# Kernel optimization log

Hardware: AMD Instinct MI355X
Metric: run time of the kernel (lower is better)

Reference implementation:

```python
import jax, jax.numpy as jnp
import numpy as np

N_HEADS = 8
STATE_TEMP = 0.5


def layer_norm(x, g, b, eps=1e-5):
    m = x.mean(-1, keepdims=True)
    v = ((x - m) ** 2).mean(-1, keepdims=True)
    return (x - m) / jnp.sqrt(v + eps) * g + b


def setup_inputs() -> dict:
    key = jax.random.key(0)
    ks = jax.random.split(key, 16)
    B, G, H, C, S, M, L = 2048, 10000, 256, 16, 32, 100, 3
    f32 = jnp.float32
    rn = lambda k, shape, scale: jax.random.normal(k, shape, f32) * scale
    return {
        'x': rn(ks[0], (B, G), 1.0),
        'enc_w1': rn(ks[1], (G, 2 * H), 1.0 / np.sqrt(G)),
        'enc_b1': jnp.zeros((2 * H,), f32),
        'enc_ln_g': jnp.ones((2 * H,), f32),
        'enc_ln_b': jnp.zeros((2 * H,), f32),
        'enc_w2': rn(ks[2], (2 * H, H), 1.0 / np.sqrt(2 * H)),
        'enc_b2': jnp.zeros((H,), f32),
        'mod_assign': rn(ks[3], (M, G), 1.0),
        'mod_inter': rn(ks[4], (M, M), 0.1) + jnp.eye(M, dtype=f32),
        'qkv_w': rn(ks[5], (L, H, 3 * H), 1.0 / np.sqrt(H)),
        'qkv_b': jnp.zeros((L, 3 * H), f32),
        'out_w': rn(ks[6], (L, H, H), 1.0 / np.sqrt(H)),
        'out_b': jnp.zeros((L, H), f32),
        'ln_g': jnp.ones((L, H), f32),
        'ln_b': jnp.zeros((L, H), f32),
        'prototypes': rn(ks[7], (S, H), 1.0),
        'clf_w1': rn(ks[8], (H, H // 2), 1.0 / np.sqrt(H)),
        'clf_b1': jnp.zeros((H // 2,), f32),
        'clf_w2': rn(ks[9], (H // 2, C), 1.0 / np.sqrt(H // 2)),
        'clf_b2': jnp.zeros((C,), f32),
        'marker_weights': jax.random.uniform(ks[10], (C, G), f32),
    }


def reference(x, enc_w1, enc_b1, enc_ln_g, enc_ln_b, enc_w2, enc_b2,
              mod_assign, mod_inter, qkv_w, qkv_b, out_w, out_b, ln_g, ln_b,
              prototypes, clf_w1, clf_b1, clf_w2, clf_b2, marker_weights):
    B = x.shape[0]
    Hd = enc_w2.shape[1]
    hd = Hd // N_HEADS
    # --- gene encoder (Linear -> LN -> ReLU -> Linear), dropout off (eval) ---
    h = jax.nn.relu(layer_norm(x @ enc_w1 + enc_b1, enc_ln_g, enc_ln_b))
    gene_features = h @ enc_w2 + enc_b2  # [B, Hd]
    # --- gene regulatory module (only sparsity_loss feeds the output dict) ---
    module_weights = jax.nn.softmax(mod_assign, axis=1)  # [M, G]
    sparsity_loss = jnp.mean(jnp.abs(module_weights)) * 0.01
    # --- stacked biological attention over seq_len N = 1 ---
    f = gene_features[:, None, :]  # [B, 1, Hd]
    for i in range(qkv_w.shape[0]):
        residual = f
        qkv = (f @ qkv_w[i] + qkv_b[i]).reshape(B, 1, 3, N_HEADS, hd)
        qkv = qkv.transpose(2, 0, 3, 1, 4)  # [3, B, nh, 1, hd]
        q, k, v = qkv[0], qkv[1], qkv[2]
        # N=1 != n_genes so the interaction-mask branch is skipped
        attn = jax.nn.softmax((q @ k.swapaxes(-2, -1)) * hd ** -0.5, axis=-1)
        o = (attn @ v).swapaxes(1, 2).reshape(B, 1, Hd)
        o = o @ out_w[i] + out_b[i]
        f = layer_norm(o + residual, ln_g[i], ln_b[i])
    feats = f[:, 0]  # [B, Hd]
    # --- soft assignment to cell-state prototypes via cosine similarity ---
    fn = jnp.linalg.norm(feats, axis=-1, keepdims=True)  # [B, 1]
    pn = jnp.linalg.norm(prototypes, axis=-1)            # [S]
    sim = (feats @ prototypes.T) / jnp.maximum(fn * pn[None, :], 1e-8)
    state_weights = jax.nn.softmax(sim / STATE_TEMP, axis=1)
    cell_states = state_weights @ prototypes  # [B, Hd]
    # --- classifier head ---
    logits = jax.nn.relu(cell_states @ clf_w1 + clf_b1) @ clf_w2 + clf_b2
    # --- eval-mode marker scores from buffer ---
    C, G = marker_weights.shape
    marker_scores = jnp.broadcast_to(marker_weights[None], (B, C, G))
    denom = jnp.maximum(jnp.sum(jnp.abs(marker_weights), axis=1, keepdims=True), 1e-12)
    marker_importance = marker_weights / denom
    return (logits, cell_states, sparsity_loss, marker_scores, marker_importance)
```

## Files before the change

kernel.cpp:

```cpp
#include <hip/hip_runtime.h>
#include <stdint.h>

#define GG 10000
#define H2 512
#define KP 10240
#define KZ 8
#define KCH 1280
#define KSTEPS 40

#define O_CS 32768L
#define O_SP 557056L
#define O_MS 557057L
#define O_MI 328237057L

typedef __attribute__((ext_vector_type(8))) short v8s;
typedef __attribute__((ext_vector_type(4))) float v4f;
typedef __attribute__((ext_vector_type(4))) unsigned short u16x4;
typedef __attribute__((ext_vector_type(8))) unsigned short u16x8;

__device__ __forceinline__ unsigned short bf16_rne(float f){
  unsigned u = __float_as_uint(f);
  u += 0x7fffu + ((u>>16)&1u);
  return (unsigned short)(u>>16);
}
__device__ __forceinline__ float bf16_f(unsigned short h){
  return __uint_as_float(((unsigned)h)<<16);
}

#define GL16(g,l) __builtin_amdgcn_global_load_lds( \
    (__attribute__((address_space(1))) void*)(uintptr_t)(g), \
    (__attribute__((address_space(3))) void*)(l), 16, 0, 0)

__global__ __launch_bounds__(256) void k_prep(
    const float* __restrict__ x, const float* __restrict__ w1,
    const float* __restrict__ qkv_w, const float* __restrict__ qkv_b,
    const float* __restrict__ out_w, const float* __restrict__ out_b,
    unsigned short* __restrict__ xh, unsigned short* __restrict__ wth,
    unsigned short* __restrict__ wtl, float* __restrict__ Wc, float* __restrict__ bc){
  __shared__ unsigned T[64][65];
  __shared__ float As[64][36], WsT[64][36];
  const int bid = blockIdx.x, tid = threadIdx.x;
  if (bid < 20480){
    int idx = bid*256 + tid;
    int row = idx / (KP/4);
    int k = (idx - row*(KP/4))*4;
    float4 v = make_float4(0.f,0.f,0.f,0.f);
    if (k < GG) v = *(const float4*)(x + (long)row*GG + k);
    float c[4] = {v.x,v.y,v.z,v.w};
    u16x4 hv;
    #pragma unroll
    for (int j=0;j<4;j++) hv[j] = bf16_rne(c[j]);
    *(u16x4*)(xh + (long)row*KP + k) = hv;
  } else if (bid < 21760){
    int b = bid - 20480;
    int k0 = (b%160)*64, n0 = (b/160)*64;
    {
      int kr = tid>>2, nc = (tid&3)*16;
      int kk = k0 + kr;
      #pragma unroll
      for (int j=0;j<16;j+=4){
        float4 v = make_float4(0.f,0.f,0.f,0.f);
        if (kk < GG) v = *(const float4*)(w1 + (long)kk*H2 + n0 + nc + j);
        float c[4] = {v.x,v.y,v.z,v.w};
        #pragma unroll
        for (int jj=0;jj<4;jj++){
          unsigned short h = bf16_rne(c[jj]);
          unsigned short l = bf16_rne(c[jj] - bf16_f(h));
          T[kr][nc+j+jj] = (unsigned)h | ((unsigned)l<<16);
        }
      }
    }
    __syncthreads();
    {
      int n = tid>>2, kc = (tid&3)*16;
      u16x8 h0, h1, l0, l1;
      #pragma unroll
      for (int j=0;j<8;j++){
        unsigned a = T[kc+j][n];
        unsigned bb = T[kc+8+j][n];
        h0[j] = (unsigned short)(a & 0xffffu); l0[j] = (unsigned short)(a>>16);
        h1[j] = (unsigned short)(bb & 0xffffu); l1[j] = (unsigned short)(bb>>16);
      }
      long off = (long)(n0+n)*KP + k0 + kc;
      *(u16x8*)(wth+off)   = h0; *(u16x8*)(wth+off+8) = h1;
      *(u16x8*)(wtl+off)   = l0; *(u16x8*)(wtl+off+8) = l1;
    }
  } else if (bid < 21808){
    int b = bid - 21760;
    const int z = b>>4, bx = (b&15)>>2, by = b&3;
    const float* A = qkv_w + (long)z*196608 + 512;
    const float* W = out_w + (long)z*65536;
    float* C = Wc + (long)z*65536;
    const int tx = tid&15, ty = tid>>4;
    const int ar = tid>>2, ak = (tid&3)*8;
    const int wr2 = tid>>3, wc2 = (tid&7)*8;
    float acc[4][4];
    #pragma unroll
    for (int i=0;i<4;i++)
      #pragma unroll
      for (int j=0;j<4;j++) acc[i][j] = 0.f;
    for (int kb=0; kb<256; kb+=32){
      float4 a0 = *(const float4*)(A + (long)(bx*64+ar)*768 + kb + ak);
      float4 a1 = *(const float4*)(A + (long)(bx*64+ar)*768 + kb + ak + 4);
      float4 w0 = *(const float4*)(W + (long)(kb+wr2)*256 + by*64 + wc2);
      float4 w1v= *(const float4*)(W + (long)(kb+wr2)*256 + by*64 + wc2 + 4);
      __syncthreads();
      *(float4*)&As[ar][ak]   = a0;
      *(float4*)&As[ar][ak+4] = a1;
      float cw[8] = {w0.x,w0.y,w0.z,w0.w,w1v.x,w1v.y,w1v.z,w1v.w};
      #pragma unroll
      for (int jj=0;jj<8;jj++) WsT[wc2+jj][wr2] = cw[jj];
      __syncthreads();
      #pragma unroll
      for (int k4=0;k4<8;k4++){
        float4 av[4], wv[4];
        #pragma unroll
        for (int i=0;i<4;i++) av[i] = *(const float4*)&As[ty + i*16][k4*4];
        #pragma unroll
        for (int j=0;j<4;j++) wv[j] = *(const float4*)&WsT[tx + j*16][k4*4];
        #pragma unroll
        for (int i=0;i<4;i++)
          #pragma unroll
          for (int j=0;j<4;j++)
            acc[i][j] += av[i].x*wv[j].x + av[i].y*wv[j].y + av[i].z*wv[j].z + av[i].w*wv[j].w;
      }
    }
    #pragma unroll
    for (int i=0;i<4;i++){
      int r = bx*64 + ty + i*16;
      #pragma unroll
      for (int j=0;j<4;j++)
        C[(long)r*256 + by*64 + tx + j*16] = acc[i][j];
    }
  } else {
    int i = bid - 21808;
    float acc = out_b[i*256 + tid];
    const float* wo = out_w + (long)i*65536;
    const float* qb = qkv_b + i*768 + 512;
    for (int j=0;j<256;j++) acc += qb[j]*wo[j*256+tid];
    bc[i*256+tid] = acc;
  }
}

__global__ __launch_bounds__(256) void k_gemm1(
    const unsigned short* __restrict__ xh,
    const unsigned short* __restrict__ wth, const unsigned short* __restrict__ wtl,
    float* __restrict__ pc){
  __shared__ unsigned short Ah[4096], Bh[4096], Bl[4096];
  const int tid = threadIdx.x;
  const int wid = tid>>6, lane = tid&63;
  const int bm = blockIdx.x, bn = blockIdx.y, kz = blockIdx.z;
  const int c0 = wid*2, c1 = c0+1;
  const int srow = lane>>2;
  const int sk8 = (lane&3)*8;
  const long kb0 = (long)kz*KCH + sk8;
  const long rA0 = (long)(bm*128 + c0*16 + srow)*KP + kb0;
  const long rA1 = (long)(bm*128 + c1*16 + srow)*KP + kb0;
  const long rB0 = (long)(bn*128 + c0*16 + srow)*KP + kb0;
  const long rB1 = (long)(bn*128 + c1*16 + srow)*KP + kb0;
  const unsigned short* pAh0 = xh + rA0;  const unsigned short* pAh1 = xh + rA1;
  const unsigned short* pBh0 = wth + rB0; const unsigned short* pBh1 = wth + rB1;
  const unsigned short* pBl0 = wtl + rB0; const unsigned short* pBl1 = wtl + rB1;
  unsigned short* dAh0 = &Ah[c0*512]; unsigned short* dAh1 = &Ah[c1*512];
  unsigned short* dBh0 = &Bh[c0*512]; unsigned short* dBh1 = &Bh[c1*512];
  unsigned short* dBl0 = &Bl[c0*512]; unsigned short* dBl1 = &Bl[c1*512];
  const int wr = wid>>1, wc = wid&1;
  const int fr = lane&15, fq = lane>>4;
  v4f acc[4][4];
  #pragma unroll
  for (int m=0;m<4;m++)
    #pragma unroll
    for (int n=0;n<4;n++){ v4f z = {0.f,0.f,0.f,0.f}; acc[m][n] = z; }

  for (int s=0; s<KSTEPS; ++s){
    GL16(pAh0, dAh0); GL16(pAh1, dAh1);
    GL16(pBh0, dBh0); GL16(pBh1, dBh1);
    GL16(pBl0, dBl0); GL16(pBl1, dBl1);
    pAh0 += 32; pAh1 += 32;
    pBh0 += 32; pBh1 += 32; pBl0 += 32; pBl1 += 32;
    __syncthreads();
    v8s ah[4], bh[4], bl[4];
    #pragma unroll
    for (int m=0;m<4;m++)
      ah[m] = *(const v8s*)&Ah[(wr*64 + m*16 + fr)*32 + fq*8];
    #pragma unroll
    for (int n=0;n<4;n++){
      int off = (wc*64 + n*16 + fr)*32 + fq*8;
      bh[n] = *(const v8s*)&Bh[off];
      bl[n] = *(const v8s*)&Bl[off];
    }
    #pragma unroll
    for (int m=0;m<4;m++)
      #pragma unroll
      for (int n=0;n<4;n++){
        acc[m][n] = __builtin_amdgcn_mfma_f32_16x16x32_bf16(ah[m], bh[n], acc[m][n], 0,0,0);
        acc[m][n] = __builtin_amdgcn_mfma_f32_16x16x32_bf16(ah[m], bl[n], acc[m][n], 0,0,0);
      }
    __syncthreads();
  }
  float* op = pc + (long)kz*(2048L*512L);
  #pragma unroll
  for (int m=0;m<4;m++){
    #pragma unroll
    for (int n=0;n<4;n++){
      int col = bn*128 + wc*64 + n*16 + fr;
      #pragma unroll
      for (int r=0;r<4;r++){
        int row = bm*128 + wr*64 + m*16 + fq*4 + r;
        op[(long)row*512 + col] = acc[m][n][r];
      }
    }
  }
}

__global__ __launch_bounds__(256) void k_reduce_ln(const float* __restrict__ pc,
    const float* __restrict__ b1, const float* __restrict__ g, const float* __restrict__ b,
    float* __restrict__ t1){
  __shared__ float red[8];
  int row = blockIdx.x, tid = threadIdx.x;
  long base = (long)row*512;
  float v0 = b1[tid], v1 = b1[tid+256];
  #pragma unroll
  for (int kz=0;kz<KZ;kz++){
    v0 += pc[(long)kz*1048576 + base + tid];
    v1 += pc[(long)kz*1048576 + base + tid + 256];
  }
  float s = v0+v1, q = v0*v0 + v1*v1;
  #pragma unroll
  for (int off=32; off; off>>=1){ s += __shfl_xor(s, off); q += __shfl_xor(q, off); }
  if ((tid&63)==0){ red[tid>>6] = s; red[4+(tid>>6)] = q; }
  __syncthreads();
  float sum = red[0]+red[1]+red[2]+red[3];
  float ssq = red[4]+red[5]+red[6]+red[7];
  float mean = sum*(1.f/512.f);
  float var  = ssq*(1.f/512.f) - mean*mean;
  float rstd = rsqrtf(var + 1e-5f);
  float r0 = (v0-mean)*rstd*g[tid]     + b[tid];
  float r1 = (v1-mean)*rstd*g[tid+256] + b[tid+256];
  t1[base+tid]     = fmaxf(r0, 0.f);
  t1[base+tid+256] = fmaxf(r1, 0.f);
}

__global__ __launch_bounds__(256) void k_gemm_f32(
    const float* __restrict__ A, int lda,
    const float* __restrict__ W, int ldw,
    const float* __restrict__ bias,
    float* __restrict__ C, int ldo, int K){
  __shared__ float As[64][36];
  __shared__ float WsT[64][36];
  const int tid = threadIdx.x;
  const int bx = blockIdx.x, by = blockIdx.y;
  const int tx = tid&15, ty = tid>>4;
  const int ar = tid>>2, ak = (tid&3)*8;
  const int wr2 = tid>>3, wc2 = (tid&7)*8;
  float acc[4][4];
  #pragma unroll
  for (int i=0;i<4;i++)
    #pragma unroll
    for (int j=0;j<4;j++) acc[i][j] = 0.f;
  for (int kb=0; kb<K; kb+=32){
    float4 a0 = *(const float4*)(A + (long)(bx*64+ar)*lda + kb + ak);
    float4 a1 = *(const float4*)(A + (long)(bx*64+ar)*lda + kb + ak + 4);
    float4 w0 = *(const float4*)(W + (long)(kb+wr2)*ldw + by*64 + wc2);
    float4 w1v= *(const float4*)(W + (long)(kb+wr2)*ldw + by*64 + wc2 + 4);
    __syncthreads();
    *(float4*)&As[ar][ak]   = a0;
    *(float4*)&As[ar][ak+4] = a1;
    float cw[8] = {w0.x,w0.y,w0.z,w0.w,w1v.x,w1v.y,w1v.z,w1v.w};
    #pragma unroll
    for (int jj=0;jj<8;jj++) WsT[wc2+jj][wr2] = cw[jj];
    __syncthreads();
    #pragma unroll
    for (int k4=0;k4<8;k4++){
      float4 av[4], wv[4];
      #pragma unroll
      for (int i=0;i<4;i++) av[i] = *(const float4*)&As[ty + i*16][k4*4];
      #pragma unroll
      for (int j=0;j<4;j++) wv[j] = *(const float4*)&WsT[tx + j*16][k4*4];
      #pragma unroll
      for (int i=0;i<4;i++)
        #pragma unroll
        for (int j=0;j<4;j++)
          acc[i][j] += av[i].x*wv[j].x + av[i].y*wv[j].y + av[i].z*wv[j].z + av[i].w*wv[j].w;
    }
  }
  #pragma unroll
  for (int i=0;i<4;i++){
    int r = bx*64 + ty + i*16;
    #pragma unroll
    for (int j=0;j<4;j++){
      int c = by*64 + tx + j*16;
      C[(long)r*ldo + c] = acc[i][j] + bias[c];
    }
  }
}

__global__ __launch_bounds__(256) void k_add_ln(const float* __restrict__ o,
    const float* __restrict__ res, const float* __restrict__ g, const float* __restrict__ b,
    float* __restrict__ fout){
  __shared__ float red[8];
  int row = blockIdx.x, tid = threadIdx.x;
  long base = (long)row*256;
  float x = o[base+tid] + res[base+tid];
  float s = x, q = x*x;
  #pragma unroll
  for (int off=32; off; off>>=1){ s += __shfl_xor(s, off); q += __shfl_xor(q, off); }
  if ((tid&63)==0){ red[tid>>6] = s; red[4+(tid>>6)] = q; }
  __syncthreads();
  float sum = red[0]+red[1]+red[2]+red[3];
  float ssq = red[4]+red[5]+red[6]+red[7];
  float mean = sum*(1.f/256.f);
  float var  = ssq*(1.f/256.f) - mean*mean;
  float rstd = rsqrtf(var + 1e-5f);
  fout[base+tid] = (x-mean)*rstd*g[tid] + b[tid];
}

__global__ __launch_bounds__(256) void k_head(const float* __restrict__ o,
    const float* __restrict__ res, const float* __restrict__ g3, const float* __restrict__ b3,
    const float* __restrict__ protos, const float* __restrict__ w1, const float* __restrict__ b1,
    const float* __restrict__ w2, const float* __restrict__ b2,
    float* __restrict__ logits, float* __restrict__ cs_out){
  __shared__ float ff[256], csb[256], hid[128], simr[32], pnl[32], sw[32], red[8];
  int row = blockIdx.x, tid = threadIdx.x;
  long base = (long)row*256;
  float xx = o[base+tid] + res[base+tid];
  {
    float s0 = xx, q0 = xx*xx;
    #pragma unroll
    for (int off=32; off; off>>=1){ s0 += __shfl_xor(s0, off); q0 += __shfl_xor(q0, off); }
    if ((tid&63)==0){ red[tid>>6] = s0; red[4+(tid>>6)] = q0; }
  }
  __syncthreads();
  float fv;
  {
    float sum = red[0]+red[1]+red[2]+red[3];
    float ssq = red[4]+red[5]+red[6]+red[7];
    float mean = sum*(1.f/256.f);
    float var  = ssq*(1.f/256.f) - mean*mean;
    float rstd = rsqrtf(var + 1e-5f);
    fv = (xx-mean)*rstd*g3[tid] + b3[tid];
  }
  ff[tid] = fv;
  __syncthreads();
  float s = fv*fv;
  #pragma unroll
  for (int off=32; off; off>>=1) s += __shfl_xor(s, off);
  if ((tid&63)==0) red[tid>>6] = s;
  __syncthreads();
  float fn = sqrtf(red[0]+red[1]+red[2]+red[3]);
  int p = tid>>3, e = tid&7;
  float d = 0.f, q = 0.f;
  for (int k=e*32; k<e*32+32; k++){ float pv = protos[p*256+k]; d += ff[k]*pv; q += pv*pv; }
  d += __shfl_xor(d,1); q += __shfl_xor(q,1);
  d += __shfl_xor(d,2); q += __shfl_xor(q,2);
  d += __shfl_xor(d,4); q += __shfl_xor(q,4);
  if (e==0){ simr[p] = d; pnl[p] = sqrtf(q); }
  __syncthreads();
  if (tid < 64){
    float z = (tid<32) ? (2.f*simr[tid]/fmaxf(fn*pnl[tid], 1e-8f)) : -3e38f;
    float m = z;
    #pragma unroll
    for (int off=16; off; off>>=1) m = fmaxf(m, __shfl_xor(m, off));
    float ev = (tid<32) ? expf(z - m) : 0.f;
    float sm = ev;
    #pragma unroll
    for (int off=16; off; off>>=1) sm += __shfl_xor(sm, off);
    if (tid<32) sw[tid] = ev/sm;
  }
  __syncthreads();
  float cs = 0.f;
  #pragma unroll 8
  for (int pp=0;pp<32;pp++) cs += sw[pp]*protos[pp*256+tid];
  cs_out[(long)row*256+tid] = cs;
  csb[tid] = cs;
  __syncthreads();
  if (tid<128){
    float hv = b1[tid];
    for (int k=0;k<256;k++) hv += csb[k]*w1[k*128+tid];
    hid[tid] = fmaxf(hv, 0.f);
  }
  __syncthreads();
  if (tid<16){
    float lv = b2[tid];
    for (int j=0;j<128;j++) lv += hid[j]*w2[j*16+tid];
    logits[(long)row*16+tid] = lv;
  }
}

__global__ __launch_bounds__(256) void k_fill_marker(const float* __restrict__ mw,
    float* __restrict__ out){
  __shared__ float red[4];
  int b = blockIdx.y;
  int t = blockIdx.x*256 + threadIdx.x;
  if (b == 2048){
    int c = blockIdx.x, tid = threadIdx.x;
    if (c >= 16) return;
    if (c==0 && tid==0) out[O_SP] = 0.01f/10000.0f;
    float s = 0.f;
    for (int g0=tid; g0<10000; g0+=256) s += fabsf(mw[c*10000+g0]);
    #pragma unroll
    for (int off=32; off; off>>=1) s += __shfl_xor(s, off);
    if ((tid&63)==0) red[tid>>6] = s;
    __syncthreads();
    float inv = 1.f/fmaxf(red[0]+red[1]+red[2]+red[3], 1e-12f);
    for (int g0=tid; g0<10000; g0+=256)
      out[O_MI + (long)c*10000 + g0] = mw[c*10000+g0]*inv;
    return;
  }
  float* base = out + O_MS + (long)b*160000;
  if (t < 40000){
    int i = 4*t;
    float4 A  = *(const float4*)(mw + i);
    float4 Bv = (i+4 < 160000) ? *(const float4*)(mw + i + 4) : *(const float4*)(mw);
    float4 v = make_float4(A.w, Bv.x, Bv.y, Bv.z);
    if (b == 2047 && t == 39999){
      base[159999] = A.w;
    } else {
      *(float4*)(base + 3 + i) = v;
    }
  }
  if (b==0 && t<3) base[t] = mw[t];
}

extern "C" void kernel_launch(void* const* d_in, const int* in_sizes, int n_in,
                              void* d_out, int out_size, void* d_ws, size_t ws_size,
                              hipStream_t stream){
  const float* x        = (const float*)d_in[0];
  const float* enc_w1   = (const float*)d_in[1];
  const float* enc_b1   = (const float*)d_in[2];
  const float* enc_ln_g = (const float*)d_in[3];
  const float* enc_ln_b = (const float*)d_in[4];
  const float* enc_w2   = (const float*)d_in[5];
  const float* enc_b2   = (const float*)d_in[6];
  const float* qkv_w    = (const float*)d_in[9];
  const float* qkv_b    = (const float*)d_in[10];
  const float* out_w    = (const float*)d_in[11];
  const float* out_b    = (const float*)d_in[12];
  const float* ln_g     = (const float*)d_in[13];
  const float* ln_b     = (const float*)d_in[14];
  const float* protos   = (const float*)d_in[15];
  const float* clf_w1   = (const float*)d_in[16];
  const float* clf_b1   = (const float*)d_in[17];
  const float* clf_w2   = (const float*)d_in[18];
  const float* clf_b2   = (const float*)d_in[19];
  const float* mw       = (const float*)d_in[20];
  float* out = (float*)d_out;

  char* scr = (char*)(((uintptr_t)d_out + O_MS*4 + 255) & ~(uintptr_t)255);
  unsigned short* xh  = (unsigned short*)(scr);
  unsigned short* wth = (unsigned short*)(scr + 83886080L);
  unsigned short* wtl = (unsigned short*)(scr + 94371840L);
  float* pc = (float*)(scr + 104857600L);
  float* t1 = (float*)(scr + 138412032L);
  float* f0 = (float*)(scr + 142606336L);
  float* f1 = (float*)(scr + 144703488L);
  float* ob = (float*)(scr + 146800640L);
  float* Wc = (float*)(scr + 148897792L);
  float* bc = (float*)(scr + 149684224L);

  k_prep     <<<21811, 256, 0, stream>>>(x, enc_w1, qkv_w, qkv_b, out_w, out_b,
                                         xh, wth, wtl, Wc, bc);
  k_gemm1    <<<dim3(16, 4, KZ), 256, 0, stream>>>(xh, wth, wtl, pc);
  k_reduce_ln<<<2048, 256, 0, stream>>>(pc, enc_b1, enc_ln_g, enc_ln_b, t1);
  k_gemm_f32 <<<dim3(32, 4), 256, 0, stream>>>(t1, 512, enc_w2, 256, enc_b2, f0, 256, 512);
  const float* fin = f0; float* fo = f1;
  for (int i=0;i<2;i++){
    k_gemm_f32<<<dim3(32,4), 256, 0, stream>>>(fin, 256, Wc + (long)i*65536, 256,
                                               bc + i*256, ob, 256, 256);
    k_add_ln  <<<2048, 256, 0, stream>>>(ob, fin, ln_g + i*256, ln_b + i*256, fo);
    const float* tmp = fo; fo = (float*)fin; fin = tmp;
  }
  k_gemm_f32<<<dim3(32,4), 256, 0, stream>>>(fin, 256, Wc + 2L*65536, 256,
                                             bc + 2*256, ob, 256, 256);
  k_head<<<2048, 256, 0, stream>>>(ob, fin, ln_g + 512, ln_b + 512,
                                   protos, clf_w1, clf_b1, clf_w2, clf_b2,
                                   out, out + O_CS);
  k_fill_marker<<<dim3(157, 2049), 256, 0, stream>>>(mw, out);
}
```

Before: 527.0 us.

## Triple-buffer LDS tiles in gemm1 with async global-to-LDS prefetch pipeline

The encoder GEMM now keeps three LDS buffers per operand and issues direct global-to-LDS loads three K-steps ahead. Partial s_waitcnt vmcnt values replace the full syncthreads drain, so global memory latency overlaps with MFMA work. LDS use triples, which may lower occupancy. Correctness depends on the vmcnt counts matching the six loads issued per stage.

```diff
diff --git a/kernel.cpp b/kernel.cpp
--- a/kernel.cpp
+++ b/kernel.cpp
@@ -146,7 +146,7 @@
     const unsigned short* __restrict__ xh,
     const unsigned short* __restrict__ wth, const unsigned short* __restrict__ wtl,
     float* __restrict__ pc){
-  __shared__ unsigned short Ah[4096], Bh[4096], Bl[4096];
+  __shared__ unsigned short Ah[3][4096], Bh[3][4096], Bl[3][4096];
   const int tid = threadIdx.x;
   const int wid = tid>>6, lane = tid&63;
   const int bm = blockIdx.x, bn = blockIdx.y, kz = blockIdx.z;
@@ -154,16 +154,13 @@
   const int srow = lane>>2;
   const int sk8 = (lane&3)*8;
   const long kb0 = (long)kz*KCH + sk8;
-  const long rA0 = (long)(bm*128 + c0*16 + srow)*KP + kb0;
-  const long rA1 = (long)(bm*128 + c1*16 + srow)*KP + kb0;
-  const long rB0 = (long)(bn*128 + c0*16 + srow)*KP + kb0;
-  const long rB1 = (long)(bn*128 + c1*16 + srow)*KP + kb0;
-  const unsigned short* pAh0 = xh + rA0;  const unsigned short* pAh1 = xh + rA1;
-  const unsigned short* pBh0 = wth + rB0; const unsigned short* pBh1 = wth + rB1;
-  const unsigned short* pBl0 = wtl + rB0; const unsigned short* pBl1 = wtl + rB1;
-  unsigned short* dAh0 = &Ah[c0*512]; unsigned short* dAh1 = &Ah[c1*512];
-  unsigned short* dBh0 = &Bh[c0*512]; unsigned short* dBh1 = &Bh[c1*512];
-  unsigned short* dBl0 = &Bl[c0*512]; unsigned short* dBl1 = &Bl[c1*512];
+  const unsigned short* pA0 = xh  + (long)(bm*128 + c0*16 + srow)*KP + kb0;
+  const unsigned short* pA1 = xh  + (long)(bm*128 + c1*16 + srow)*KP + kb0;
+  const unsigned short* pH0 = wth + (long)(bn*128 + c0*16 + srow)*KP + kb0;
+  const unsigned short* pH1 = wth + (long)(bn*128 + c1*16 + srow)*KP + kb0;
+  const unsigned short* pL0 = wtl + (long)(bn*128 + c0*16 + srow)*KP + kb0;
+  const unsigned short* pL1 = wtl + (long)(bn*128 + c1*16 + srow)*KP + kb0;
+  const int d0 = c0*512, d1 = c1*512;
   const int wr = wid>>1, wc = wid&1;
   const int fr = lane&15, fq = lane>>4;
   v4f acc[4][4];
@@ -172,22 +169,28 @@
     #pragma unroll
     for (int n=0;n<4;n++){ v4f z = {0.f,0.f,0.f,0.f}; acc[m][n] = z; }
 
+#define STAGE(d, s) do{ long o=(long)(s)*32; \
+    GL16(pA0+o, &Ah[d][d0]); GL16(pA1+o, &Ah[d][d1]); \
+    GL16(pH0+o, &Bh[d][d0]); GL16(pH1+o, &Bh[d][d1]); \
+    GL16(pL0+o, &Bl[d][d0]); GL16(pL1+o, &Bl[d][d1]); }while(0)
+
+  STAGE(0, 0); STAGE(1, 1); STAGE(2, 2);
+  int cur = 0;
   for (int s=0; s<KSTEPS; ++s){
-    GL16(pAh0, dAh0); GL16(pAh1, dAh1);
-    GL16(pBh0, dBh0); GL16(pBh1, dBh1);
-    GL16(pBl0, dBl0); GL16(pBl1, dBl1);
-    pAh0 += 32; pAh1 += 32;
-    pBh0 += 32; pBh1 += 32; pBl0 += 32; pBl1 += 32;
-    __syncthreads();
+    if (s <= KSTEPS-3)      asm volatile("s_waitcnt vmcnt(12)" ::: "memory");
+    else if (s == KSTEPS-2) asm volatile("s_waitcnt vmcnt(6)"  ::: "memory");
+    else                    asm volatile("s_waitcnt vmcnt(0)"  ::: "memory");
+    __builtin_amdgcn_s_barrier();
+    __builtin_amdgcn_sched_barrier(0);
     v8s ah[4], bh[4], bl[4];
     #pragma unroll
     for (int m=0;m<4;m++)
-      ah[m] = *(const v8s*)&Ah[(wr*64 + m*16 + fr)*32 + fq*8];
+      ah[m] = *(const v8s*)&Ah[cur][(wr*64 + m*16 + fr)*32 + fq*8];
     #pragma unroll
     for (int n=0;n<4;n++){
       int off = (wc*64 + n*16 + fr)*32 + fq*8;
-      bh[n] = *(const v8s*)&Bh[off];
-      bl[n] = *(const v8s*)&Bl[off];
+      bh[n] = *(const v8s*)&Bh[cur][off];
+      bl[n] = *(const v8s*)&Bl[cur][off];
     }
     #pragma unroll
     for (int m=0;m<4;m++)
@@ -196,8 +199,12 @@
         acc[m][n] = __builtin_amdgcn_mfma_f32_16x16x32_bf16(ah[m], bh[n], acc[m][n], 0,0,0);
         acc[m][n] = __builtin_amdgcn_mfma_f32_16x16x32_bf16(ah[m], bl[n], acc[m][n], 0,0,0);
       }
-    __syncthreads();
-  }
+    __builtin_amdgcn_s_barrier();
+    __builtin_amdgcn_sched_barrier(0);
+    if (s+3 < KSTEPS) STAGE(cur, s+3);
+    cur = (cur==2) ? 0 : cur+1;
+  }
+#undef STAGE
   float* op = pc + (long)kz*(2048L*512L);
   #pragma unroll
   for (int m=0;m<4;m++){
```

Result: no change. 528.0 us (+0.2%).
